# Kernel optimization log

Measured on AMD Instinct MI355X. Metric: run time of the kernel, lower is better.

The kernel has to match this reference:

```python
import jax, jax.numpy as jnp
import numpy as np

NU, N1, N2 = 100000, 60000, 60000   # users, domain-1 items, domain-2 items
E = 2000000                          # click edges per domain
DIN, DH, DOUT = 128, 128, 64


def setup_inputs() -> dict:
    key = jax.random.key(0)
    ks = jax.random.split(key, 14)
    emb = lambda k, shape: jax.random.normal(k, shape, dtype=jnp.float32) * 0.01
    w = lambda k, shape: jax.random.normal(k, shape, dtype=jnp.float32) * (1.0 / np.sqrt(shape[-2]))
    return {
        "emb_user": emb(ks[0], (NU, DIN)),
        "emb_d1": emb(ks[1], (N1, DIN)),
        "emb_d2": emb(ks[2], (N2, DIN)),
        # relation order: [user->d1 click, d1->user rev, user->d2 click, d2->user rev]
        "W_in": w(ks[3], (4, DIN, DH)),
        "b_in": jnp.zeros((4, DH), jnp.float32),
        "W_hid": w(ks[4], (4, DH, DH)),
        "b_hid": jnp.zeros((4, DH), jnp.float32),
        "W_out": w(ks[5], (4, DH, DOUT)),
        "b_out": jnp.zeros((4, DOUT), jnp.float32),
        "Wp_d1": jax.random.normal(ks[6], (DOUT, DOUT), dtype=jnp.float32),
        "Wp_d2": jax.random.normal(ks[7], (DOUT, DOUT), dtype=jnp.float32),
        "src_d1": jax.random.randint(ks[8], (E,), 0, NU, dtype=jnp.int32),
        "dst_d1": jax.random.randint(ks[9], (E,), 0, N1, dtype=jnp.int32),
        "src_d2": jax.random.randint(ks[10], (E,), 0, NU, dtype=jnp.int32),
        "dst_d2": jax.random.randint(ks[11], (E,), 0, N2, dtype=jnp.int32),
    }


def _gconv(x_src, W, b, src, dst, nsrc, ndst, n_dst):
    # DGL GraphConv, norm='both': D_dst^{-1/2} A D_src^{-1/2} (X W) + b
    m = (x_src * nsrc[:, None]) @ W                      # [N_src, dout]
    agg = jax.ops.segment_sum(m[src], dst, num_segments=n_dst)  # SpMM via gather/scatter
    return agg * ndst[:, None] + b


def reference(emb_user, emb_d1, emb_d2, W_in, b_in, W_hid, b_hid, W_out, b_out,
              Wp_d1, Wp_d2, src_d1, dst_d1, src_d2, dst_d2):
    Nu, Na, Nb = emb_user.shape[0], emb_d1.shape[0], emb_d2.shape[0]
    ones1 = jnp.ones(src_d1.shape[0], jnp.float32)
    ones2 = jnp.ones(src_d2.shape[0], jnp.float32)
    du1 = jax.ops.segment_sum(ones1, src_d1, num_segments=Nu)
    di1 = jax.ops.segment_sum(ones1, dst_d1, num_segments=Na)
    du2 = jax.ops.segment_sum(ones2, src_d2, num_segments=Nu)
    di2 = jax.ops.segment_sum(ones2, dst_d2, num_segments=Nb)
    r = lambda d: jax.lax.rsqrt(jnp.maximum(d, 1.0))
    nu1, ni1, nu2, ni2 = r(du1), r(di1), r(du2), r(di2)

    u, i1, i2 = emb_user, emb_d1, emb_d2
    layers = ((W_in, b_in, False), (W_hid, b_hid, False), (W_out, b_out, True))
    for W, b, last in layers:
        # HeteroGraphConv with aggregate='sum': user receives from both reverse relations
        u_new = (_gconv(i1, W[1], b[1], dst_d1, src_d1, ni1, nu1, Nu)
                 + _gconv(i2, W[3], b[3], dst_d2, src_d2, ni2, nu2, Nu))
        i1_new = _gconv(u, W[0], b[0], src_d1, dst_d1, nu1, ni1, Na)
        i2_new = _gconv(u, W[2], b[2], src_d2, dst_d2, nu2, ni2, Nb)
        if last:
            u, i1, i2 = u_new, i1_new, i2_new
        else:  # relu + dropout (eval mode: dropout is identity)
            u, i1, i2 = jax.nn.relu(u_new), jax.nn.relu(i1_new), jax.nn.relu(i2_new)

    # per-domain projection of user embeddings, then u_dot_v edge scoring
    u1 = u @ Wp_d1
    u2 = u @ Wp_d2
    s1 = jnp.sum(u1[src_d1] * i1[dst_d1], axis=-1)  # [E]
    s2 = jnp.sum(u2[src_d2] * i2[dst_d2], axis=-1)  # [E]
    return jnp.concatenate([s1, s2])
```

## Files before the change

### kernel.cpp

```cpp
#include <hip/hip_runtime.h>
#include <hip/hip_bf16.h>

typedef unsigned short ushort_t;
typedef __attribute__((ext_vector_type(8))) short bf16x8;
typedef __attribute__((ext_vector_type(4))) float f32x4;

constexpr int NU = 100000, N1 = 60000, N2 = 60000;
constexpr int E = 2000000;
constexpr int TOTN = 2 * NU + N1 + N2;
constexpr int NPART = 8;
constexpr int CH = 2048;
constexpr int NCHUNKS = (E + CH - 1) / CH;
constexpr int PSLICE = TOTN / NPART;
constexpr int NSUB = 8;
constexpr int SUBS = PSLICE / NSUB;

__device__ __forceinline__ ushort_t f2bf(float f) {
  unsigned u = __float_as_uint(f);
  u = u + 0x7fffu + ((u >> 16) & 1u);
  return (ushort_t)(u >> 16);
}

__global__ __launch_bounds__(256) void k_count(const int* __restrict__ s1,
                                               const int* __restrict__ d1,
                                               const int* __restrict__ s2,
                                               const int* __restrict__ d2,
                                               int* __restrict__ deg) {
  __shared__ int ls1[CH], ld1[CH], ls2[CH], ld2[CH];
  int part = blockIdx.x % NPART;
  int base = (blockIdx.x / NPART) * CH;
  int n = E - base; if (n > CH) n = CH;
  for (int i = threadIdx.x; i < n; i += 256) {
    ls1[i] = s1[base + i];
    ld1[i] = d1[base + i];
    ls2[i] = s2[base + i];
    ld2[i] = d2[base + i];
  }
  __syncthreads();
  int plo = part * PSLICE;
  for (int sub = 0; sub < NSUB; ++sub) {
    int lo = plo + sub * SUBS, hi = lo + SUBS;
    for (int i = threadIdx.x; i < n; i += 256) {
      int i0 = ls1[i];
      int i1 = NU + ld1[i];
      int i2 = NU + N1 + ls2[i];
      int i3 = 2 * NU + N1 + ld2[i];
      if (i0 >= lo && i0 < hi) atomicAdd(&deg[i0], 1);
      if (i1 >= lo && i1 < hi) atomicAdd(&deg[i1], 1);
      if (i2 >= lo && i2 < hi) atomicAdd(&deg[i2], 1);
      if (i3 >= lo && i3 < hi) atomicAdd(&deg[i3], 1);
    }
    __syncthreads();
  }
}

__global__ __launch_bounds__(256) void k_norm(const int* __restrict__ deg,
                                              float* __restrict__ nrm) {
  int i = blockIdx.x * 256 + threadIdx.x;
  if (i >= TOTN) return;
  int d = deg[i];
  nrm[i] = rsqrtf((float)(d > 1 ? d : 1));
}

__global__ __launch_bounds__(256) void k_scan(const int* __restrict__ deg,
                                              int* __restrict__ off,
                                              int* __restrict__ cur) {
  __shared__ int wsum[4];
  int seg = blockIdx.x;
  int baseIn, n, baseOut;
  if (seg == 0)      { baseIn = 0;            n = NU; baseOut = 0; }
  else if (seg == 1) { baseIn = NU;           n = N1; baseOut = NU + 1; }
  else if (seg == 2) { baseIn = NU + N1;      n = NU; baseOut = NU + N1 + 2; }
  else               { baseIn = 2 * NU + N1;  n = N2; baseOut = 2 * NU + N1 + 3; }
  const int* in = deg + baseIn;
  int* out = off + baseOut;
  int* curp = cur + baseIn;

  constexpr int ITEMS = 16;
  int t = threadIdx.x, lane = t & 63, wid = t >> 6;
  int carry = 0;
  for (int base = 0; base < n; base += 256 * ITEMS) {
    int vals[ITEMS];
    int lsum = 0;
    int i0 = base + t * ITEMS;
#pragma unroll
    for (int j = 0; j < ITEMS; ++j) {
      int i = i0 + j;
      int v = (i < n) ? in[i] : 0;
      vals[j] = v;
      lsum += v;
    }
    int incl = lsum;
#pragma unroll
    for (int d = 1; d < 64; d <<= 1) {
      int x = __shfl_up(incl, d, 64);
      if (lane >= d) incl += x;
    }
    if (lane == 63) wsum[wid] = incl;
    __syncthreads();
    int woff = 0;
    for (int w = 0; w < wid; ++w) woff += wsum[w];
    int chunkTotal = wsum[0] + wsum[1] + wsum[2] + wsum[3];
    int excl = carry + woff + (incl - lsum);
#pragma unroll
    for (int j = 0; j < ITEMS; ++j) {
      int i = i0 + j;
      if (i < n) { out[i] = excl; curp[i] = excl; }
      excl += vals[j];
    }
    carry += chunkTotal;
    __syncthreads();
  }
  if (t == 0) out[n] = carry;
}

__global__ __launch_bounds__(256) void k_fill(const int* __restrict__ s1,
                                              const int* __restrict__ d1,
                                              const int* __restrict__ s2,
                                              const int* __restrict__ d2,
                                              int* __restrict__ cur,
                                              int* __restrict__ a_s1,
                                              int* __restrict__ a_d1,
                                              int* __restrict__ a_s2,
                                              int* __restrict__ a_d2,
                                              int* __restrict__ e_s1,
                                              int* __restrict__ e_s2) {
  __shared__ int ls1[CH], ld1[CH], ls2[CH], ld2[CH];
  int part = blockIdx.x % NPART;
  int base = (blockIdx.x / NPART) * CH;
  int n = E - base; if (n > CH) n = CH;
  for (int i = threadIdx.x; i < n; i += 256) {
    ls1[i] = s1[base + i];
    ld1[i] = d1[base + i];
    ls2[i] = s2[base + i];
    ld2[i] = d2[base + i];
  }
  __syncthreads();
  int plo = part * PSLICE;
  for (int sub = 0; sub < NSUB; ++sub) {
    int lo = plo + sub * SUBS, hi = lo + SUBS;
    for (int i = threadIdx.x; i < n; i += 256) {
      int a = ls1[i], b = ld1[i];
      int i0 = a, i1 = NU + b;
      if (i0 >= lo && i0 < hi) {
        int pos = atomicAdd(&cur[i0], 1);
        a_s1[pos] = b;
        e_s1[pos] = base + i;
      }
      if (i1 >= lo && i1 < hi) a_d1[atomicAdd(&cur[i1], 1)] = a;
      int c = ls2[i], d = ld2[i];
      int i2 = NU + N1 + c, i3 = 2 * NU + N1 + d;
      if (i2 >= lo && i2 < hi) {
        int pos = atomicAdd(&cur[i2], 1);
        a_s2[pos] = d;
        e_s2[pos] = base + i;
      }
      if (i3 >= lo && i3 < hi) a_d2[atomicAdd(&cur[i3], 1)] = c;
    }
    __syncthreads();
  }
}

__device__ __forceinline__ bf16x8 loadA8(const float* p) {
  float4 lo = *(const float4*)p;
  float4 hi = *(const float4*)(p + 4);
  bf16x8 v;
  v[0] = (short)f2bf(lo.x); v[1] = (short)f2bf(lo.y);
  v[2] = (short)f2bf(lo.z); v[3] = (short)f2bf(lo.w);
  v[4] = (short)f2bf(hi.x); v[5] = (short)f2bf(hi.y);
  v[6] = (short)f2bf(hi.z); v[7] = (short)f2bf(hi.w);
  return v;
}
__device__ __forceinline__ bf16x8 loadA8(const ushort_t* p) {
  return *(const bf16x8*)p;
}

template <typename AT, int K, int N, bool BF16OUT>
__global__ __launch_bounds__(256) void k_gemm(const AT* __restrict__ A,
                                              const float* __restrict__ W,
                                              void* __restrict__ Cv, int M,
                                              const float* __restrict__ rowscale) {
  constexpr int KF = K / 32, NF = N / 16;
  __shared__ __align__(16) ushort_t sW[N * K];
  for (int i = threadIdx.x * 4; i < K * N; i += 1024) {
    float4 w4 = *(const float4*)&W[i];
    int k = i / N, n0 = i % N;
    float wv[4] = {w4.x, w4.y, w4.z, w4.w};
#pragma unroll
    for (int j = 0; j < 4; ++j) {
      int n = n0 + j;
      sW[(n * K + k) ^ ((n & 7) << 3)] = f2bf(wv[j]);
    }
  }
  __syncthreads();

  int w = threadIdx.x >> 6, lane = threadIdx.x & 63;
  int col = lane & 15, kg = lane >> 4;
  int r = blockIdx.x * 64 + w * 16 + col;
  int rA = r < M ? r : M - 1;

  bf16x8 af[KF];
#pragma unroll
  for (int kf = 0; kf < KF; ++kf)
    af[kf] = loadA8(&A[(size_t)rA * K + kf * 32 + kg * 8]);

  f32x4 acc[NF] = {};
#pragma unroll
  for (int nf = 0; nf < NF; ++nf) {
    int n = nf * 16 + col;
#pragma unroll
    for (int kf = 0; kf < KF; ++kf) {
      int idx = (n * K + kf * 32 + kg * 8) ^ ((n & 7) << 3);
      bf16x8 bfrag = *(const bf16x8*)&sW[idx];
      acc[nf] = __builtin_amdgcn_mfma_f32_16x16x32_bf16(af[kf], bfrag, acc[nf], 0, 0, 0);
    }
  }

  int orow = blockIdx.x * 64 + w * 16 + kg * 4;
#pragma unroll
  for (int reg = 0; reg < 4; ++reg) {
    int R = orow + reg;
    if (R >= M) break;
    float sc = rowscale ? rowscale[R] : 1.f;
#pragma unroll
    for (int nf = 0; nf < NF; ++nf) {
      float v = sc * acc[nf][reg];
      size_t o = (size_t)R * N + nf * 16 + col;
      if constexpr (BF16OUT) ((ushort_t*)Cv)[o] = f2bf(v);
      else                   ((float*)Cv)[o] = v;
    }
  }
}

template <int D>
__device__ __forceinline__ void accum_list(const ushort_t* __restrict__ z,
                                           const int* __restrict__ adj,
                                           int e0, int e1, int l, float4& A) {
  auto addp = [&](uint2 p) {
    A.x += __uint_as_float(p.x << 16);
    A.y += __uint_as_float(p.x & 0xffff0000u);
    A.z += __uint_as_float(p.y << 16);
    A.w += __uint_as_float(p.y & 0xffff0000u);
  };
  int e = e0;
  for (; e + 4 <= e1; e += 4) {
    int sA = adj[e], sB = adj[e + 1], sC = adj[e + 2], sD = adj[e + 3];
    uint2 pA = *(const uint2*)&z[(size_t)sA * D + 4 * l];
    uint2 pB = *(const uint2*)&z[(size_t)sB * D + 4 * l];
    uint2 pC = *(const uint2*)&z[(size_t)sC * D + 4 * l];
    uint2 pD = *(const uint2*)&z[(size_t)sD * D + 4 * l];
    addp(pA); addp(pB); addp(pC); addp(pD);
  }
  for (; e < e1; ++e)
    addp(*(const uint2*)&z[(size_t)adj[e] * D + 4 * l]);
}

template <int D, bool RELU, bool BF16OUT>
__global__ __launch_bounds__(256) void k_gather(const ushort_t* __restrict__ z,
                                                const int* __restrict__ off,
                                                const int* __restrict__ adj,
                                                const float* __restrict__ ndst,
                                                const float* __restrict__ bias,
                                                void* __restrict__ outv, int nv) {
  constexpr int LPN = D / 4;
  constexpr int NPB = 256 / LPN;
  int t = threadIdx.x;
  int slot = t / LPN, l = t % LPN;
  int v = blockIdx.x * NPB + slot;
  if (v >= nv) return;
  float4 A = {0.f, 0.f, 0.f, 0.f};
  accum_list<D>(z, adj, off[v], off[v + 1], l, A);
  float nd = ndst[v];
  float r0 = nd * A.x + bias[4 * l];
  float r1 = nd * A.y + bias[4 * l + 1];
  float r2 = nd * A.z + bias[4 * l + 2];
  float r3 = nd * A.w + bias[4 * l + 3];
  if constexpr (RELU) {
    r0 = fmaxf(r0, 0.f); r1 = fmaxf(r1, 0.f);
    r2 = fmaxf(r2, 0.f); r3 = fmaxf(r3, 0.f);
  }
  size_t o = (size_t)v * D + 4 * l;
  if constexpr (BF16OUT) {
    uint2 pk;
    pk.x = (unsigned)f2bf(r0) | ((unsigned)f2bf(r1) << 16);
    pk.y = (unsigned)f2bf(r2) | ((unsigned)f2bf(r3) << 16);
    *(uint2*)&((ushort_t*)outv)[o] = pk;
  } else {
    float4 res; res.x = r0; res.y = r1; res.z = r2; res.w = r3;
    *(float4*)&((float*)outv)[o] = res;
  }
}

template <int D, bool RELU>
__global__ __launch_bounds__(256) void k_gather2(const ushort_t* __restrict__ z1,
                                                 const ushort_t* __restrict__ z2,
                                                 const int* __restrict__ off1,
                                                 const int* __restrict__ adj1,
                                                 const int* __restrict__ off2,
                                                 const int* __restrict__ adj2,
                                                 const float* __restrict__ nd1,
                                                 const float* __restrict__ nd2,
                                                 const float* __restrict__ b1,
                                                 const float* __restrict__ b2,
                                                 ushort_t* __restrict__ out, int nv) {
  constexpr int LPN = D / 4;
  constexpr int NPB = 256 / LPN;
  int t = threadIdx.x;
  int slot = t / LPN, l = t % LPN;
  int v = blockIdx.x * NPB + slot;
  if (v >= nv) return;
  float4 A = {0.f, 0.f, 0.f, 0.f};
  float4 B = {0.f, 0.f, 0.f, 0.f};
  accum_list<D>(z1, adj1, off1[v], off1[v + 1], l, A);
  accum_list<D>(z2, adj2, off2[v], off2[v + 1], l, B);
  float n1 = nd1[v], n2 = nd2[v];
  float r0 = n1 * A.x + n2 * B.x + b1[4 * l]     + b2[4 * l];
  float r1 = n1 * A.y + n2 * B.y + b1[4 * l + 1] + b2[4 * l + 1];
  float r2 = n1 * A.z + n2 * B.z + b1[4 * l + 2] + b2[4 * l + 2];
  float r3 = n1 * A.w + n2 * B.w + b1[4 * l + 3] + b2[4 * l + 3];
  if constexpr (RELU) {
    r0 = fmaxf(r0, 0.f); r1 = fmaxf(r1, 0.f);
    r2 = fmaxf(r2, 0.f); r3 = fmaxf(r3, 0.f);
  }
  uint2 pk;
  pk.x = (unsigned)f2bf(r0) | ((unsigned)f2bf(r1) << 16);
  pk.y = (unsigned)f2bf(r2) | ((unsigned)f2bf(r3) << 16);
  *(uint2*)&out[(size_t)v * D + 4 * l] = pk;
}

__global__ __launch_bounds__(256) void k_score2(const float* __restrict__ up,
                                                const float* __restrict__ ip,
                                                const int* __restrict__ off,
                                                const int* __restrict__ adj,
                                                const int* __restrict__ eid,
                                                float* __restrict__ out, int nu) {
  int w = threadIdx.x >> 6, lane = threadIdx.x & 63;
  int u = blockIdx.x * 4 + w;
  if (u >= nu) return;
  float uc = up[(size_t)u * 64 + lane];
  int e0 = off[u], e1 = off[u + 1];
  int e = e0;
  for (; e + 2 <= e1; e += 2) {
    int sA = adj[e], sB = adj[e + 1];
    int idA = eid[e], idB = eid[e + 1];
    float pA = uc * ip[(size_t)sA * 64 + lane];
    float pB = uc * ip[(size_t)sB * 64 + lane];
#pragma unroll
    for (int d = 32; d >= 1; d >>= 1) {
      pA += __shfl_xor(pA, d, 64);
      pB += __shfl_xor(pB, d, 64);
    }
    if (lane == 0) { out[idA] = pA; out[idB] = pB; }
  }
  if (e < e1) {
    int s = adj[e], id = eid[e];
    float p = uc * ip[(size_t)s * 64 + lane];
#pragma unroll
    for (int d = 32; d >= 1; d >>= 1) p += __shfl_xor(p, d, 64);
    if (lane == 0) out[id] = p;
  }
}

extern "C" void kernel_launch(void* const* d_in, const int* in_sizes, int n_in,
                              void* d_out, int out_size, void* d_ws, size_t ws_size,
                              hipStream_t stream) {
  const float* emb_user = (const float*)d_in[0];
  const float* emb_d1   = (const float*)d_in[1];
  const float* emb_d2   = (const float*)d_in[2];
  const float* W_in     = (const float*)d_in[3];
  const float* b_in     = (const float*)d_in[4];
  const float* W_hid    = (const float*)d_in[5];
  const float* b_hid    = (const float*)d_in[6];
  const float* W_out    = (const float*)d_in[7];
  const float* b_out    = (const float*)d_in[8];
  const float* Wp_d1    = (const float*)d_in[9];
  const float* Wp_d2    = (const float*)d_in[10];
  const int* src_d1     = (const int*)d_in[11];
  const int* dst_d1     = (const int*)d_in[12];
  const int* src_d2     = (const int*)d_in[13];
  const int* dst_d2     = (const int*)d_in[14];
  float* out = (float*)d_out;

  char* p = (char*)d_ws;
  auto alloc = [&](size_t bytes) {
    void* r = (void*)p;
    p += (bytes + 15) & ~(size_t)15;
    return r;
  };
  ushort_t* bufU[2] = {(ushort_t*)alloc((size_t)NU * 128 * 2),
                       (ushort_t*)alloc((size_t)NU * 128 * 2)};
  void* bufI1 = alloc((size_t)N1 * 128 * 2);
  void* bufI2 = alloc((size_t)N2 * 128 * 2);
  ushort_t* m = (ushort_t*)alloc((size_t)(N1 + N2) * 128 * 2);
  float* nrm = (float*)alloc((size_t)TOTN * 4);
  int* deg = (int*)alloc((size_t)TOTN * 4);
  int* off = (int*)alloc((size_t)(TOTN + 4) * 4);
  int* cur = (int*)alloc((size_t)TOTN * 4);
  int* adj_s1 = (int*)alloc((size_t)E * 4);
  int* adj_d1 = (int*)alloc((size_t)E * 4);
  int* adj_s2 = (int*)alloc((size_t)E * 4);
  int* adj_d2 = (int*)alloc((size_t)E * 4);
  int* eid_s1 = (int*)alloc((size_t)E * 4);
  int* eid_s2 = (int*)alloc((size_t)E * 4);

  if ((size_t)(p - (char*)d_ws) > ws_size) return;

  const float* nu1 = nrm;
  const float* ni1 = nrm + NU;
  const float* nu2 = nrm + NU + N1;
  const float* ni2 = nrm + 2 * NU + N1;
  const int* off_u1 = off;
  const int* off_i1 = off + NU + 1;
  const int* off_u2 = off + NU + N1 + 2;
  const int* off_i2 = off + 2 * NU + N1 + 3;

  hipMemsetAsync(deg, 0, (size_t)TOTN * 4, stream);
  k_count<<<NCHUNKS * NPART, 256, 0, stream>>>(src_d1, dst_d1, src_d2, dst_d2, deg);
  k_norm<<<(TOTN + 255) / 256, 256, 0, stream>>>(deg, nrm);
  k_scan<<<4, 256, 0, stream>>>(deg, off, cur);
  k_fill<<<NCHUNKS * NPART, 256, 0, stream>>>(src_d1, dst_d1, src_d2, dst_d2, cur,
                                              adj_s1, adj_d1, adj_s2, adj_d2,
                                              eid_s1, eid_s2);

  ushort_t* mI1 = m;
  ushort_t* mI2 = m + (size_t)N1 * 128;
  ushort_t* mI1h = m;
  ushort_t* mI2h = m + (size_t)N1 * 64;
  ushort_t* mU = m;

  k_gemm<float, 128, 128, true><<<(N1 + 63) / 64, 256, 0, stream>>>(emb_d1, W_in + 1 * 128 * 128, mI1, N1, ni1);
  k_gemm<float, 128, 128, true><<<(N2 + 63) / 64, 256, 0, stream>>>(emb_d2, W_in + 3 * 128 * 128, mI2, N2, ni2);
  k_gather2<128, true><<<(NU + 7) / 8, 256, 0, stream>>>(
      mI1, mI2, off_u1, adj_s1, off_u2, adj_s2, nu1, nu2,
      b_in + 1 * 128, b_in + 3 * 128, bufU[0], NU);
  k_gemm<float, 128, 128, true><<<(NU + 63) / 64, 256, 0, stream>>>(emb_user, W_in + 0 * 128 * 128, mU, NU, nu1);
  k_gather<128, true, true><<<(N1 + 7) / 8, 256, 0, stream>>>(
      mU, off_i1, adj_d1, ni1, b_in + 0 * 128, bufI1, N1);
  k_gemm<float, 128, 128, true><<<(NU + 63) / 64, 256, 0, stream>>>(emb_user, W_in + 2 * 128 * 128, mU, NU, nu2);
  k_gather<128, true, true><<<(N2 + 7) / 8, 256, 0, stream>>>(
      mU, off_i2, adj_d2, ni2, b_in + 2 * 128, bufI2, N2);

  k_gemm<ushort_t, 128, 128, true><<<(N1 + 63) / 64, 256, 0, stream>>>((ushort_t*)bufI1, W_hid + 1 * 128 * 128, mI1, N1, ni1);
  k_gemm<ushort_t, 128, 128, true><<<(N2 + 63) / 64, 256, 0, stream>>>((ushort_t*)bufI2, W_hid + 3 * 128 * 128, mI2, N2, ni2);
  k_gather2<128, true><<<(NU + 7) / 8, 256, 0, stream>>>(
      mI1, mI2, off_u1, adj_s1, off_u2, adj_s2, nu1, nu2,
      b_hid + 1 * 128, b_hid + 3 * 128, bufU[1], NU);
  k_gemm<ushort_t, 128, 128, true><<<(NU + 63) / 64, 256, 0, stream>>>(bufU[0], W_hid + 0 * 128 * 128, mU, NU, nu1);
  k_gather<128, true, true><<<(N1 + 7) / 8, 256, 0, stream>>>(
      mU, off_i1, adj_d1, ni1, b_hid + 0 * 128, bufI1, N1);
  k_gemm<ushort_t, 128, 128, true><<<(NU + 63) / 64, 256, 0, stream>>>(bufU[0], W_hid + 2 * 128 * 128, mU, NU, nu2);
  k_gather<128, true, true><<<(N2 + 7) / 8, 256, 0, stream>>>(
      mU, off_i2, adj_d2, ni2, b_hid + 2 * 128, bufI2, N2);

  k_gemm<ushort_t, 128, 64, true><<<(N1 + 63) / 64, 256, 0, stream>>>((ushort_t*)bufI1, W_out + 1 * 128 * 64, mI1h, N1, ni1);
  k_gemm<ushort_t, 128, 64, true><<<(N2 + 63) / 64, 256, 0, stream>>>((ushort_t*)bufI2, W_out + 3 * 128 * 64, mI2h, N2, ni2);
  k_gather2<64, false><<<(NU + 15) / 16, 256, 0, stream>>>(
      mI1h, mI2h, off_u1, adj_s1, off_u2, adj_s2, nu1, nu2,
      b_out + 1 * 64, b_out + 3 * 64, bufU[0], NU);
  k_gemm<ushort_t, 128, 64, true><<<(NU + 63) / 64, 256, 0, stream>>>(bufU[1], W_out + 0 * 128 * 64, mU, NU, nu1);
  k_gather<64, false, false><<<(N1 + 15) / 16, 256, 0, stream>>>(
      mU, off_i1, adj_d1, ni1, b_out + 0 * 64, bufI1, N1);
  k_gemm<ushort_t, 128, 64, true><<<(NU + 63) / 64, 256, 0, stream>>>(bufU[1], W_out + 2 * 128 * 64, mU, NU, nu2);
  k_gather<64, false, false><<<(N2 + 15) / 16, 256, 0, stream>>>(
      mU, off_i2, adj_d2, ni2, b_out + 2 * 64, bufI2, N2);

  float* u1 = (float*)m;
  float* u2 = (float*)bufU[1];
  k_gemm<ushort_t, 64, 64, false><<<(NU + 63) / 64, 256, 0, stream>>>(bufU[0], Wp_d1, u1, NU, nullptr);
  k_gemm<ushort_t, 64, 64, false><<<(NU + 63) / 64, 256, 0, stream>>>(bufU[0], Wp_d2, u2, NU, nullptr);
  k_score2<<<(NU + 3) / 4, 256, 0, stream>>>(u1, (const float*)bufI1, off_u1, adj_s1, eid_s1, out, NU);
  k_score2<<<(NU + 3) / 4, 256, 0, stream>>>(u2, (const float*)bufI2, off_u2, adj_s2, eid_s2, out + E, NU);
}
```

Baseline: 2.386 ms.

## Interleave adjacency with edge ids, fuse projection into scoring, restructure CSR fill

The CSR fill kernel now reads edges straight from global memory with a larger chunk and spreads sub-ranges across blocks instead of looping over them inside one block. User-side adjacency and edge ids are stored together as int2. The per-domain user projection GEMM is folded into the scoring kernel through shared-memory Wp and wave shuffles, which removes two GEMM launches and the fp32 u1/u2 round trip. The gather inner loop is unrolled to 8 outstanding loads. In exchange the int2 layout doubles index bandwidth in the gather2 kernels, fill2 rereads edge arrays once per sub-range block, and the projection matvec now runs from bf16 inputs.

```diff
diff --git a/kernel.cpp b/kernel.cpp
--- a/kernel.cpp
+++ b/kernel.cpp
@@ -14,11 +14,18 @@
 constexpr int PSLICE = TOTN / NPART;
 constexpr int NSUB = 8;
 constexpr int SUBS = PSLICE / NSUB;
+constexpr int CH2 = 8192;
+constexpr int NCH2 = (E + CH2 - 1) / CH2;
+constexpr int NSUB2 = 4;
+constexpr int SUBS2 = PSLICE / NSUB2;
 
 __device__ __forceinline__ ushort_t f2bf(float f) {
   unsigned u = __float_as_uint(f);
   u = u + 0x7fffu + ((u >> 16) & 1u);
   return (ushort_t)(u >> 16);
+}
+__device__ __forceinline__ float bf2f(ushort_t v) {
+  return __uint_as_float(((unsigned)v) << 16);
 }
 
 __global__ __launch_bounds__(256) void k_count(const int* __restrict__ s1,
@@ -114,50 +121,37 @@
   if (t == 0) out[n] = carry;
 }
 
-__global__ __launch_bounds__(256) void k_fill(const int* __restrict__ s1,
-                                              const int* __restrict__ d1,
-                                              const int* __restrict__ s2,
-                                              const int* __restrict__ d2,
-                                              int* __restrict__ cur,
-                                              int* __restrict__ a_s1,
-                                              int* __restrict__ a_d1,
-                                              int* __restrict__ a_s2,
-                                              int* __restrict__ a_d2,
-                                              int* __restrict__ e_s1,
-                                              int* __restrict__ e_s2) {
-  __shared__ int ls1[CH], ld1[CH], ls2[CH], ld2[CH];
+__global__ __launch_bounds__(256) void k_fill2(const int* __restrict__ s1,
+                                               const int* __restrict__ d1,
+                                               const int* __restrict__ s2,
+                                               const int* __restrict__ d2,
+                                               int* __restrict__ cur,
+                                               int2* __restrict__ ae_s1,
+                                               int* __restrict__ a_d1,
+                                               int2* __restrict__ ae_s2,
+                                               int* __restrict__ a_d2) {
   int part = blockIdx.x % NPART;
-  int base = (blockIdx.x / NPART) * CH;
-  int n = E - base; if (n > CH) n = CH;
-  for (int i = threadIdx.x; i < n; i += 256) {
-    ls1[i] = s1[base + i];
-    ld1[i] = d1[base + i];
-    ls2[i] = s2[base + i];
-    ld2[i] = d2[base + i];
-  }
-  __syncthreads();
-  int plo = part * PSLICE;
-  for (int sub = 0; sub < NSUB; ++sub) {
-    int lo = plo + sub * SUBS, hi = lo + SUBS;
-    for (int i = threadIdx.x; i < n; i += 256) {
-      int a = ls1[i], b = ld1[i];
-      int i0 = a, i1 = NU + b;
-      if (i0 >= lo && i0 < hi) {
-        int pos = atomicAdd(&cur[i0], 1);
-        a_s1[pos] = b;
-        e_s1[pos] = base + i;
-      }
-      if (i1 >= lo && i1 < hi) a_d1[atomicAdd(&cur[i1], 1)] = a;
-      int c = ls2[i], d = ld2[i];
-      int i2 = NU + N1 + c, i3 = 2 * NU + N1 + d;
-      if (i2 >= lo && i2 < hi) {
-        int pos = atomicAdd(&cur[i2], 1);
-        a_s2[pos] = d;
-        e_s2[pos] = base + i;
-      }
-      if (i3 >= lo && i3 < hi) a_d2[atomicAdd(&cur[i3], 1)] = c;
-    }
-    __syncthreads();
+  int chunk = (blockIdx.x / NPART) % NCH2;
+  int sub = blockIdx.x / (NPART * NCH2);
+  int lo = part * PSLICE + sub * SUBS2, hi = lo + SUBS2;
+  int base = chunk * CH2;
+  int end = base + CH2 < E ? base + CH2 : E;
+  for (int i = base + threadIdx.x; i < end; i += 256) {
+    int a = s1[i], b = d1[i];
+    if (a >= lo && a < hi) {
+      int pos = atomicAdd(&cur[a], 1);
+      ae_s1[pos] = make_int2(b, i);
+    }
+    int i1 = NU + b;
+    if (i1 >= lo && i1 < hi) a_d1[atomicAdd(&cur[i1], 1)] = a;
+    int c = s2[i], d = d2[i];
+    int i2 = NU + N1 + c;
+    if (i2 >= lo && i2 < hi) {
+      int pos = atomicAdd(&cur[i2], 1);
+      ae_s2[pos] = make_int2(d, i);
+    }
+    int i3 = 2 * NU + N1 + d;
+    if (i3 >= lo && i3 < hi) a_d2[atomicAdd(&cur[i3], 1)] = c;
   }
 }
 
@@ -232,9 +226,12 @@
   }
 }
 
-template <int D>
+__device__ __forceinline__ int adj_idx(int v) { return v; }
+__device__ __forceinline__ int adj_idx(int2 v) { return v.x; }
+
+template <int D, typename IdxT>
 __device__ __forceinline__ void accum_list(const ushort_t* __restrict__ z,
-                                           const int* __restrict__ adj,
+                                           const IdxT* __restrict__ adj,
                                            int e0, int e1, int l, float4& A) {
   auto addp = [&](uint2 p) {
     A.x += __uint_as_float(p.x << 16);
@@ -243,16 +240,16 @@
     A.w += __uint_as_float(p.y & 0xffff0000u);
   };
   int e = e0;
-  for (; e + 4 <= e1; e += 4) {
-    int sA = adj[e], sB = adj[e + 1], sC = adj[e + 2], sD = adj[e + 3];
-    uint2 pA = *(const uint2*)&z[(size_t)sA * D + 4 * l];
-    uint2 pB = *(const uint2*)&z[(size_t)sB * D + 4 * l];
-    uint2 pC = *(const uint2*)&z[(size_t)sC * D + 4 * l];
-    uint2 pD = *(const uint2*)&z[(size_t)sD * D + 4 * l];
-    addp(pA); addp(pB); addp(pC); addp(pD);
+  for (; e + 8 <= e1; e += 8) {
+    uint2 p[8];
+#pragma unroll
+    for (int j = 0; j < 8; ++j)
+      p[j] = *(const uint2*)&z[(size_t)adj_idx(adj[e + j]) * D + 4 * l];
+#pragma unroll
+    for (int j = 0; j < 8; ++j) addp(p[j]);
   }
   for (; e < e1; ++e)
-    addp(*(const uint2*)&z[(size_t)adj[e] * D + 4 * l]);
+    addp(*(const uint2*)&z[(size_t)adj_idx(adj[e]) * D + 4 * l]);
 }
 
 template <int D, bool RELU, bool BF16OUT>
@@ -295,9 +292,9 @@
 __global__ __launch_bounds__(256) void k_gather2(const ushort_t* __restrict__ z1,
                                                  const ushort_t* __restrict__ z2,
                                                  const int* __restrict__ off1,
-                                                 const int* __restrict__ adj1,
+                                                 const int2* __restrict__ ae1,
                                                  const int* __restrict__ off2,
-                                                 const int* __restrict__ adj2,
+                                                 const int2* __restrict__ ae2,
                                                  const float* __restrict__ nd1,
                                                  const float* __restrict__ nd2,
                                                  const float* __restrict__ b1,
@@ -311,8 +308,8 @@
   if (v >= nv) return;
   float4 A = {0.f, 0.f, 0.f, 0.f};
   float4 B = {0.f, 0.f, 0.f, 0.f};
-  accum_list<D>(z1, adj1, off1[v], off1[v + 1], l, A);
-  accum_list<D>(z2, adj2, off2[v], off2[v + 1], l, B);
+  accum_list<D>(z1, ae1, off1[v], off1[v + 1], l, A);
+  accum_list<D>(z2, ae2, off2[v], off2[v + 1], l, B);
   float n1 = nd1[v], n2 = nd2[v];
   float r0 = n1 * A.x + n2 * B.x + b1[4 * l]     + b2[4 * l];
   float r1 = n1 * A.y + n2 * B.y + b1[4 * l + 1] + b2[4 * l + 1];
@@ -328,36 +325,45 @@
   *(uint2*)&out[(size_t)v * D + 4 * l] = pk;
 }
 
-__global__ __launch_bounds__(256) void k_score2(const float* __restrict__ up,
+__global__ __launch_bounds__(256) void k_score2(const ushort_t* __restrict__ u64,
+                                                const float* __restrict__ Wp,
                                                 const float* __restrict__ ip,
                                                 const int* __restrict__ off,
-                                                const int* __restrict__ adj,
-                                                const int* __restrict__ eid,
+                                                const int2* __restrict__ ae,
                                                 float* __restrict__ out, int nu) {
+  __shared__ float sWp[64 * 64];
+  for (int i = threadIdx.x * 4; i < 4096; i += 1024)
+    *(float4*)&sWp[i] = *(const float4*)&Wp[i];
+  __syncthreads();
   int w = threadIdx.x >> 6, lane = threadIdx.x & 63;
   int u = blockIdx.x * 4 + w;
   if (u >= nu) return;
-  float uc = up[(size_t)u * 64 + lane];
+  float x = bf2f(u64[(size_t)u * 64 + lane]);
+  float p = 0.f;
+#pragma unroll
+  for (int c = 0; c < 64; ++c) {
+    float xc = __shfl(x, c, 64);
+    p += xc * sWp[c * 64 + lane];
+  }
   int e0 = off[u], e1 = off[u + 1];
   int e = e0;
   for (; e + 2 <= e1; e += 2) {
-    int sA = adj[e], sB = adj[e + 1];
-    int idA = eid[e], idB = eid[e + 1];
-    float pA = uc * ip[(size_t)sA * 64 + lane];
-    float pB = uc * ip[(size_t)sB * 64 + lane];
+    int2 A = ae[e], B = ae[e + 1];
+    float pA = p * ip[(size_t)A.x * 64 + lane];
+    float pB = p * ip[(size_t)B.x * 64 + lane];
 #pragma unroll
     for (int d = 32; d >= 1; d >>= 1) {
       pA += __shfl_xor(pA, d, 64);
       pB += __shfl_xor(pB, d, 64);
     }
-    if (lane == 0) { out[idA] = pA; out[idB] = pB; }
+    if (lane == 0) { out[A.y] = pA; out[B.y] = pB; }
   }
   if (e < e1) {
-    int s = adj[e], id = eid[e];
-    float p = uc * ip[(size_t)s * 64 + lane];
-#pragma unroll
-    for (int d = 32; d >= 1; d >>= 1) p += __shfl_xor(p, d, 64);
-    if (lane == 0) out[id] = p;
+    int2 A = ae[e];
+    float pA = p * ip[(size_t)A.x * 64 + lane];
+#pragma unroll
+    for (int d = 32; d >= 1; d >>= 1) pA += __shfl_xor(pA, d, 64);
+    if (lane == 0) out[A.y] = pA;
   }
 }
 
@@ -396,12 +402,10 @@
   int* deg = (int*)alloc((size_t)TOTN * 4);
   int* off = (int*)alloc((size_t)(TOTN + 4) * 4);
   int* cur = (int*)alloc((size_t)TOTN * 4);
-  int* adj_s1 = (int*)alloc((size_t)E * 4);
+  int2* ae_s1 = (int2*)alloc((size_t)E * 8);
   int* adj_d1 = (int*)alloc((size_t)E * 4);
-  int* adj_s2 = (int*)alloc((size_t)E * 4);
+  int2* ae_s2 = (int2*)alloc((size_t)E * 8);
   int* adj_d2 = (int*)alloc((size_t)E * 4);
-  int* eid_s1 = (int*)alloc((size_t)E * 4);
-  int* eid_s2 = (int*)alloc((size_t)E * 4);
 
   if ((size_t)(p - (char*)d_ws) > ws_size) return;
 
@@ -418,9 +422,8 @@
   k_count<<<NCHUNKS * NPART, 256, 0, stream>>>(src_d1, dst_d1, src_d2, dst_d2, deg);
   k_norm<<<(TOTN + 255) / 256, 256, 0, stream>>>(deg, nrm);
   k_scan<<<4, 256, 0, stream>>>(deg, off, cur);
-  k_fill<<<NCHUNKS * NPART, 256, 0, stream>>>(src_d1, dst_d1, src_d2, dst_d2, cur,
-                                              adj_s1, adj_d1, adj_s2, adj_d2,
-                                              eid_s1, eid_s2);
+  k_fill2<<<NSUB2 * NCH2 * NPART, 256, 0, stream>>>(src_d1, dst_d1, src_d2, dst_d2, cur,
+                                                    ae_s1, adj_d1, ae_s2, adj_d2);
 
   ushort_t* mI1 = m;
   ushort_t* mI2 = m + (size_t)N1 * 128;
@@ -431,7 +434,7 @@
   k_gemm<float, 128, 128, true><<<(N1 + 63) / 64, 256, 0, stream>>>(emb_d1, W_in + 1 * 128 * 128, mI1, N1, ni1);
   k_gemm<float, 128, 128, true><<<(N2 + 63) / 64, 256, 0, stream>>>(emb_d2, W_in + 3 * 128 * 128, mI2, N2, ni2);
   k_gather2<128, true><<<(NU + 7) / 8, 256, 0, stream>>>(
-      mI1, mI2, off_u1, adj_s1, off_u2, adj_s2, nu1, nu2,
+      mI1, mI2, off_u1, ae_s1, off_u2, ae_s2, nu1, nu2,
       b_in + 1 * 128, b_in + 3 * 128, bufU[0], NU);
   k_gemm<float, 128, 128, true><<<(NU + 63) / 64, 256, 0, stream>>>(emb_user, W_in + 0 * 128 * 128, mU, NU, nu1);
   k_gather<128, true, true><<<(N1 + 7) / 8, 256, 0, stream>>>(
@@ -443,7 +446,7 @@
   k_gemm<ushort_t, 128, 128, true><<<(N1 + 63) / 64, 256, 0, stream>>>((ushort_t*)bufI1, W_hid + 1 * 128 * 128, mI1, N1, ni1);
   k_gemm<ushort_t, 128, 128, true><<<(N2 + 63) / 64, 256, 0, stream>>>((ushort_t*)bufI2, W_hid + 3 * 128 * 128, mI2, N2, ni2);
   k_gather2<128, true><<<(NU + 7) / 8, 256, 0, stream>>>(
-      mI1, mI2, off_u1, adj_s1, off_u2, adj_s2, nu1, nu2,
+      mI1, mI2, off_u1, ae_s1, off_u2, ae_s2, nu1, nu2,
       b_hid + 1 * 128, b_hid + 3 * 128, bufU[1], NU);
   k_gemm<ushort_t, 128, 128, true><<<(NU + 63) / 64, 256, 0, stream>>>(bufU[0], W_hid + 0 * 128 * 128, mU, NU, nu1);
   k_gather<128, true, true><<<(N1 + 7) / 8, 256, 0, stream>>>(
@@ -455,7 +458,7 @@
   k_gemm<ushort_t, 128, 64, true><<<(N1 + 63) / 64, 256, 0, stream>>>((ushort_t*)bufI1, W_out + 1 * 128 * 64, mI1h, N1, ni1);
   k_gemm<ushort_t, 128, 64, true><<<(N2 + 63) / 64, 256, 0, stream>>>((ushort_t*)bufI2, W_out + 3 * 128 * 64, mI2h, N2, ni2);
   k_gather2<64, false><<<(NU + 15) / 16, 256, 0, stream>>>(
-      mI1h, mI2h, off_u1, adj_s1, off_u2, adj_s2, nu1, nu2,
+      mI1h, mI2h, off_u1, ae_s1, off_u2, ae_s2, nu1, nu2,
       b_out + 1 * 64, b_out + 3 * 64, bufU[0], NU);
   k_gemm<ushort_t, 128, 64, true><<<(NU + 63) / 64, 256, 0, stream>>>(bufU[1], W_out + 0 * 128 * 64, mU, NU, nu1);
   k_gather<64, false, false><<<(N1 + 15) / 16, 256, 0, stream>>>(
@@ -464,10 +467,8 @@
   k_gather<64, false, false><<<(N2 + 15) / 16, 256, 0, stream>>>(
       mU, off_i2, adj_d2, ni2, b_out + 2 * 64, bufI2, N2);
 
-  float* u1 = (float*)m;
-  float* u2 = (float*)bufU[1];
-  k_gemm<ushort_t, 64, 64, false><<<(NU + 63) / 64, 256, 0, stream>>>(bufU[0], Wp_d1, u1, NU, nullptr);
-  k_gemm<ushort_t, 64, 64, false><<<(NU + 63) / 64, 256, 0, stream>>>(bufU[0], Wp_d2, u2, NU, nullptr);
-  k_score2<<<(NU + 3) / 4, 256, 0, stream>>>(u1, (const float*)bufI1, off_u1, adj_s1, eid_s1, out, NU);
-  k_score2<<<(NU + 3) / 4, 256, 0, stream>>>(u2, (const float*)bufI2, off_u2, adj_s2, eid_s2, out + E, NU);
-}
+  k_score2<<<(NU + 3) / 4, 256, 0, stream>>>(bufU[0], Wp_d1, (const float*)bufI1,
+                                             off_u1, ae_s1, out, NU);
+  k_score2<<<(NU + 3) / 4, 256, 0, stream>>>(bufU[0], Wp_d2, (const float*)bufI2,
+                                             off_u2, ae_s2, out + E, NU);
+}
```

Result: slower. 2.470 ms (+3.5%).
